# Kernel tuning notes

Measured on AMD Instinct MI355X. Metric: run time of the kernel, lower is better.

## Reference

```python
import jax, jax.numpy as jnp
import numpy as np
import math

B, T, C, N = 2, 2048, 1024, 16  # batch, seq, h_dim, n_heads
D = C // N                      # head dim = 64


def setup_inputs() -> dict:
    key = jax.random.key(0)
    ks = jax.random.split(key, 9)
    s = 1.0 / math.sqrt(C)
    x = jax.random.normal(ks[0], (B, T, C), dtype=jnp.float32)
    Wq = jax.random.normal(ks[1], (C, C), dtype=jnp.float32) * s
    Wk = jax.random.normal(ks[2], (C, C), dtype=jnp.float32) * s
    Wv = jax.random.normal(ks[3], (C, C), dtype=jnp.float32) * s
    Wp = jax.random.normal(ks[4], (C, C), dtype=jnp.float32) * s
    bq = jax.random.normal(ks[5], (C,), dtype=jnp.float32) * 0.01
    bk = jax.random.normal(ks[6], (C,), dtype=jnp.float32) * 0.01
    bv = jax.random.normal(ks[7], (C,), dtype=jnp.float32) * 0.01
    bp = jax.random.normal(ks[8], (C,), dtype=jnp.float32) * 0.01
    mask = jnp.tril(jnp.ones((T, T), dtype=jnp.int32))[None, None]  # [1,1,T,T] causal
    return {"x": x, "Wq": Wq, "bq": bq, "Wk": Wk, "bk": bk,
            "Wv": Wv, "bv": bv, "Wp": Wp, "bp": bp, "mask": mask}


def reference(x, Wq, bq, Wk, bk, Wv, bv, Wp, bp, mask):
    b, t, c = x.shape
    n, d = N, c // N
    # projections; rearrange 'b t (n d) -> b n t d'
    q = (x @ Wq + bq).reshape(b, t, n, d).transpose(0, 2, 1, 3)
    k = (x @ Wk + bk).reshape(b, t, n, d).transpose(0, 2, 1, 3)
    v = (x @ Wv + bv).reshape(b, t, n, d).transpose(0, 2, 1, 3)
    # source: (q @ k^T).transpose(2,3) -> weights[b,n,i,j] = q_j . k_i (TRANSPOSED scores)
    weights = jnp.einsum('bntd,bnsd->bnst', q, k) / math.sqrt(d)
    weights = jnp.where(mask == 0, -jnp.inf, weights)
    attn = jax.nn.softmax(weights, axis=-1)          # softmax over query index j
    out = jnp.einsum('bnij,bnjd->bnid', attn, v)     # [b,n,t,d]
    out = out.transpose(0, 2, 1, 3).reshape(b, t, c)
    return out @ Wp + bp
```

## Files before the change

kernel.cpp:

```cpp
#include <hip/hip_runtime.h>
#include <hip/hip_bf16.h>

#define TT 2048
#define NHD 16

typedef __attribute__((ext_vector_type(8))) short bf16x8;
typedef __attribute__((ext_vector_type(4))) float f32x4;
typedef __attribute__((ext_vector_type(8))) unsigned short us8;
typedef __attribute__((ext_vector_type(4))) unsigned short us4;

typedef __attribute__((address_space(1))) void gvoid;
typedef __attribute__((address_space(3))) void svoid;

__device__ __forceinline__ void gll16(const void* g, void* l) {
    __builtin_amdgcn_global_load_lds((gvoid*)g, (svoid*)l, 16, 0, 0);
}

__device__ __forceinline__ unsigned short f2bf(float f) {
    union { float f; unsigned u; } v; v.f = f;
    unsigned r = v.u + 0x7fffu + ((v.u >> 16) & 1u);
    return (unsigned short)(r >> 16);
}
__device__ __forceinline__ float bf2f(unsigned short u) {
    union { unsigned u; float f; } v; v.u = ((unsigned)u) << 16;
    return v.f;
}

#define MFMA16(a, b, c) __builtin_amdgcn_mfma_f32_16x16x32_bf16((a), (b), (c), 0, 0, 0)

__global__ __launch_bounds__(256) void convert_x(const float* __restrict__ x,
                                                 unsigned short* __restrict__ xh,
                                                 unsigned short* __restrict__ xl) {
    const int i = blockIdx.x * 256 + threadIdx.x;
    const float4 a = ((const float4*)x)[2 * i];
    const float4 b = ((const float4*)x)[2 * i + 1];
    const float v[8] = {a.x, a.y, a.z, a.w, b.x, b.y, b.z, b.w};
    us8 H, L;
    #pragma unroll
    for (int j = 0; j < 8; ++j) {
        const unsigned short h = f2bf(v[j]);
        H[j] = h;
        L[j] = f2bf(v[j] - bf2f(h));
    }
    ((us8*)xh)[i] = H;
    ((us8*)xl)[i] = L;
}

__global__ __launch_bounds__(256) void convert_w(const float* __restrict__ W,
                                                 unsigned short* __restrict__ Wh,
                                                 unsigned short* __restrict__ Wl) {
    __shared__ float tile[32 * 33];
    const int t = threadIdx.x;
    const int k0 = blockIdx.x * 32, n0 = blockIdx.y * 32;

    const int kl_ = t >> 3, nc = (t & 7) * 4;
    const float4 v = *(const float4*)&W[(size_t)(k0 + kl_) * 1024 + n0 + nc];
    tile[(nc + 0) * 33 + kl_] = v.x;
    tile[(nc + 1) * 33 + kl_] = v.y;
    tile[(nc + 2) * 33 + kl_] = v.z;
    tile[(nc + 3) * 33 + kl_] = v.w;
    __syncthreads();
    const int nl = t >> 3, kc = (t & 7) * 4;
    us4 H, L;
    #pragma unroll
    for (int j = 0; j < 4; ++j) {
        const float f = tile[nl * 33 + kc + j];
        const unsigned short h = f2bf(f);
        H[j] = h;
        L[j] = f2bf(f - bf2f(h));
    }
    *(us4*)&Wh[(size_t)(n0 + nl) * 1024 + k0 + kc] = H;
    *(us4*)&Wl[(size_t)(n0 + nl) * 1024 + k0 + kc] = L;
}

template <int OUTMODE>
__global__ __launch_bounds__(256, 3)
void proj_gemm(const unsigned short* __restrict__ Ah, const unsigned short* __restrict__ Al,
               const unsigned short* __restrict__ Bh, const unsigned short* __restrict__ Bl,
               const float* __restrict__ bias,
               unsigned short* __restrict__ Oh, unsigned short* __restrict__ Ol,
               float* __restrict__ Of) {
    __shared__ __align__(16) unsigned short sm[24576];
    unsigned short* sAh = sm;
    unsigned short* sAl = sm + 8192;
    unsigned short* sBh = sm + 16384;
    unsigned short* sBl = sm + 20480;

    const int t = threadIdx.x;
    const int lane = t & 63, w = t >> 6;
    const int wr = w >> 1, wc = w & 1;
    const int l15 = lane & 15, lq = lane >> 4;
    const int row0 = blockIdx.x * 128;
    const int col0 = blockIdx.y * 64;

    f32x4 acc[4][2] = {};

    for (int k0 = 0; k0 < 1024; k0 += 64) {
        __syncthreads();
        #pragma unroll
        for (int cc = 0; cc < 4; ++cc) {
            const int c = w * 4 + cc;
            const int r = 8 * c + (lane >> 3);
            const int src = (row0 + r) * 1024 + k0 + 8 * ((lane & 7) ^ (r & 7));
            gll16(&Ah[src], &sAh[c * 512]);
            gll16(&Al[src], &sAl[c * 512]);
        }
        #pragma unroll
        for (int cc = 0; cc < 2; ++cc) {
            const int c = w * 2 + cc;
            const int r = 8 * c + (lane >> 3);
            const int src = (col0 + r) * 1024 + k0 + 8 * ((lane & 7) ^ (r & 7));
            gll16(&Bh[src], &sBh[c * 512]);
            gll16(&Bl[src], &sBl[c * 512]);
        }
        __syncthreads();
        #pragma unroll
        for (int kh = 0; kh < 2; ++kh) {
            bf16x8 aH[4], aL[4], bH[2], bL[2];
            #pragma unroll
            for (int nt = 0; nt < 2; ++nt) {
                const int rn = 32 * wc + 16 * nt + l15;
                const int off = rn * 64 + 8 * ((lq + 4 * kh) ^ (rn & 7));
                bH[nt] = *(const bf16x8*)&sBh[off];
                bL[nt] = *(const bf16x8*)&sBl[off];
            }
            #pragma unroll
            for (int mt = 0; mt < 4; ++mt) {
                const int rm = 64 * wr + 16 * mt + l15;
                const int off = rm * 64 + 8 * ((lq + 4 * kh) ^ (rm & 7));
                aH[mt] = *(const bf16x8*)&sAh[off];
                aL[mt] = *(const bf16x8*)&sAl[off];
            }
            #pragma unroll
            for (int mt = 0; mt < 4; ++mt)
                #pragma unroll
                for (int nt = 0; nt < 2; ++nt) {
                    acc[mt][nt] = MFMA16(aH[mt], bH[nt], acc[mt][nt]);
                    acc[mt][nt] = MFMA16(aH[mt], bL[nt], acc[mt][nt]);
                    acc[mt][nt] = MFMA16(aL[mt], bH[nt], acc[mt][nt]);
                }
        }
    }

    __syncthreads();
    float* sc = (float*)sm + w * (64 * 36);
    #pragma unroll
    for (int mt = 0; mt < 4; ++mt)
        #pragma unroll
        for (int nt = 0; nt < 2; ++nt) {
            const float bsv = bias[col0 + 32 * wc + 16 * nt + l15];
            #pragma unroll
            for (int r = 0; r < 4; ++r)
                sc[(16 * mt + 4 * lq + r) * 36 + 16 * nt + l15] = acc[mt][nt][r] + bsv;
        }
    asm volatile("" ::: "memory");
    #pragma unroll
    for (int rr = 0; rr < 4; ++rr) {
        const int rl = 16 * rr + (lane >> 2);
        const int c8 = (lane & 3) * 8;
        const float4 f0 = *(const float4*)&sc[rl * 36 + c8];
        const float4 f1 = *(const float4*)&sc[rl * 36 + c8 + 4];
        const float v[8] = {f0.x, f0.y, f0.z, f0.w, f1.x, f1.y, f1.z, f1.w};
        const int gr = row0 + 64 * wr + rl;
        const int gc = col0 + 32 * wc + c8;
        if (OUTMODE == 2) {
            *(float4*)&Of[(size_t)gr * 1024 + gc] = f0;
            *(float4*)&Of[(size_t)gr * 1024 + gc + 4] = f1;
        } else {
            us8 H, L;
            #pragma unroll
            for (int j = 0; j < 8; ++j) {
                const unsigned short h = f2bf(v[j]);
                H[j] = h;
                L[j] = f2bf(v[j] - bf2f(h));
            }
            *(us8*)&Oh[(size_t)gr * 1024 + gc] = H;
            if (OUTMODE == 0) *(us8*)&Ol[(size_t)gr * 1024 + gc] = L;
        }
    }
}

__global__ __launch_bounds__(256, 3)
void attn_mfma(const unsigned short* __restrict__ Qh_, const unsigned short* __restrict__ Ql_,
               const unsigned short* __restrict__ Kh_, const unsigned short* __restrict__ Kl_,
               const unsigned short* __restrict__ Vh_,
               unsigned short* __restrict__ Oh, unsigned short* __restrict__ Ol) {
    __shared__ __align__(16) unsigned short sm[24576];
    unsigned short* sQh = sm;
    unsigned short* sQl = sm + 4096;
    unsigned short* sKh = sm + 8192;
    unsigned short* sKl = sm + 12288;
    unsigned short* sVt = sm + 16384;
    unsigned short* sP  = sm + 20480;

    const int t = threadIdx.x;
    const int lane = t & 63, w = t >> 6;
    const int l15 = lane & 15, lq = lane >> 4;
    const int bn = blockIdx.x;
    const int b = bn >> 4, n = bn & 15;
    const int qt = (gridDim.y - 1) - blockIdx.y;
    const int rowQ0 = b * TT + qt * 64;
    const int colh = n * 64;

    #pragma unroll
    for (int cc = 0; cc < 2; ++cc) {
        const int c = w * 2 + cc;
        const int r = 8 * c + (lane >> 3);
        const int src = (rowQ0 + r) * 1024 + colh + 8 * ((lane & 7) ^ (r & 7));
        gll16(&Qh_[src], &sQh[c * 512]);
        gll16(&Ql_[src], &sQl[c * 512]);
    }

    float m_[4], l_[4];
    f32x4 o[4] = {};
    #pragma unroll
    for (int r = 0; r < 4; ++r) { m_[r] = -1e30f; l_[r] = 0.f; }

    for (int kt = 0; kt <= qt; ++kt) {
        const int rowK0 = b * TT + kt * 64;
        __syncthreads();
        #pragma unroll
        for (int cc = 0; cc < 2; ++cc) {
            const int c = w * 2 + cc;
            const int r = 8 * c + (lane >> 3);
            const int src = (rowK0 + r) * 1024 + colh + 8 * ((lane & 7) ^ (r & 7));
            gll16(&Kh_[src], &sKh[c * 512]);
            gll16(&Kl_[src], &sKl[c * 512]);
        }
        {
            const int d = lane;
            unsigned pk[8];
            #pragma unroll
            for (int ip = 0; ip < 8; ++ip) {
                const int j0 = 16 * w + 2 * ip;
                const unsigned short v0 = Vh_[(rowK0 + j0) * 1024 + colh + d];
                const unsigned short v1 = Vh_[(rowK0 + j0 + 1) * 1024 + colh + d];
                pk[ip] = (unsigned)v0 | ((unsigned)v1 << 16);
            }
            unsigned* VtI = (unsigned*)sVt;
            #pragma unroll
            for (int ip = 0; ip < 8; ++ip) {
                const int slot = 2 * w + (ip >> 2);
                VtI[d * 32 + 4 * (slot ^ (d & 7)) + (ip & 3)] = pk[ip];
            }
        }
        __syncthreads();

        f32x4 s[4] = {};
        const int njt = (kt == qt) ? (w + 1) : 4;
        #pragma unroll
        for (int kh = 0; kh < 2; ++kh) {
            const int rq = 16 * w + l15;
            const int offq = rq * 64 + 8 * ((lq + 4 * kh) ^ (rq & 7));
            const bf16x8 qH = *(const bf16x8*)&sQh[offq];
            const bf16x8 qL = *(const bf16x8*)&sQl[offq];
            #pragma unroll
            for (int jt = 0; jt < 4; ++jt) {
                if (jt >= njt) continue;
                const int rk = 16 * jt + l15;
                const int offk = rk * 64 + 8 * ((lq + 4 * kh) ^ (rk & 7));
                const bf16x8 kH = *(const bf16x8*)&sKh[offk];
                const bf16x8 kL = *(const bf16x8*)&sKl[offk];
                s[jt] = MFMA16(qH, kH, s[jt]);
                s[jt] = MFMA16(qH, kL, s[jt]);
                s[jt] = MFMA16(qL, kH, s[jt]);
            }
        }
        if (kt == qt) {
            #pragma unroll
            for (int jt = 0; jt < 4; ++jt)
                #pragma unroll
                for (int r = 0; r < 4; ++r)
                    if (16 * jt + l15 > 16 * w + 4 * lq + r) s[jt][r] = -1e30f;
        }

        float po[4][4];
        #pragma unroll
        for (int r = 0; r < 4; ++r) {
            float mx = fmaxf(fmaxf(s[0][r], s[1][r]), fmaxf(s[2][r], s[3][r]));
            #pragma unroll
            for (int off = 8; off; off >>= 1) mx = fmaxf(mx, __shfl_xor(mx, off, 16));
            const float mnew = fmaxf(m_[r], mx);
            const float alpha = __expf((m_[r] - mnew) * 0.125f);
            m_[r] = mnew;
            float ps = 0.f;
            #pragma unroll
            for (int jt = 0; jt < 4; ++jt) {
                const float p = __expf((s[jt][r] - mnew) * 0.125f);
                po[r][jt] = p;
                ps += p;
            }
            #pragma unroll
            for (int off = 8; off; off >>= 1) ps += __shfl_xor(ps, off, 16);
            l_[r] = l_[r] * alpha + ps;
            #pragma unroll
            for (int dt = 0; dt < 4; ++dt) o[dt][r] *= alpha;
        }
        unsigned short* Pw = sP + w * 1024;
        #pragma unroll
        for (int r = 0; r < 4; ++r) {
            const int rl = 4 * lq + r;
            #pragma unroll
            for (int jt = 0; jt < 4; ++jt) {
                const int c = 16 * jt + l15;
                Pw[rl * 64 + 8 * ((c >> 3) ^ (rl & 7)) + (c & 7)] = f2bf(po[r][jt]);
            }
        }
        __syncthreads();

        #pragma unroll
        for (int kh = 0; kh < 2; ++kh) {
            const int offp = l15 * 64 + 8 * ((lq + 4 * kh) ^ (l15 & 7));
            const bf16x8 pa = *(const bf16x8*)&Pw[offp];
            #pragma unroll
            for (int dt = 0; dt < 4; ++dt) {
                const int rd = 16 * dt + l15;
                const int offv = rd * 64 + 8 * ((lq + 4 * kh) ^ (rd & 7));
                const bf16x8 vb = *(const bf16x8*)&sVt[offv];
                o[dt] = MFMA16(pa, vb, o[dt]);
            }
        }
    }

    float inv[4];
    #pragma unroll
    for (int r = 0; r < 4; ++r) inv[r] = 1.0f / l_[r];
    float* sc = (float*)sm + w * (16 * 68);
    #pragma unroll
    for (int dt = 0; dt < 4; ++dt)
        #pragma unroll
        for (int r = 0; r < 4; ++r)
            sc[(4 * lq + r) * 68 + 16 * dt + l15] = o[dt][r] * inv[r];
    asm volatile("" ::: "memory");
    #pragma unroll
    for (int it = 0; it < 2; ++it) {
        const int rl = 8 * it + (lane >> 3);
        const int c8 = (lane & 7) * 8;
        const float4 f0 = *(const float4*)&sc[rl * 68 + c8];
        const float4 f1 = *(const float4*)&sc[rl * 68 + c8 + 4];
        const float v[8] = {f0.x, f0.y, f0.z, f0.w, f1.x, f1.y, f1.z, f1.w};
        us8 H, L;
        #pragma unroll
        for (int j = 0; j < 8; ++j) {
            const unsigned short h = f2bf(v[j]);
            H[j] = h;
            L[j] = f2bf(v[j] - bf2f(h));
        }
        const int gt = rowQ0 + 16 * w + rl;
        *(us8*)&Oh[(size_t)gt * 1024 + colh + c8] = H;
        *(us8*)&Ol[(size_t)gt * 1024 + colh + c8] = L;
    }
}

extern "C" void kernel_launch(void* const* d_in, const int* in_sizes, int n_in,
                              void* d_out, int out_size, void* d_ws, size_t ws_size,
                              hipStream_t stream) {
    const float* x  = (const float*)d_in[0];
    const float* Wq = (const float*)d_in[1];
    const float* bq = (const float*)d_in[2];
    const float* Wk = (const float*)d_in[3];
    const float* bk = (const float*)d_in[4];
    const float* Wv = (const float*)d_in[5];
    const float* bv = (const float*)d_in[6];
    const float* Wp = (const float*)d_in[7];
    const float* bp = (const float*)d_in[8];
    float* out = (float*)d_out;

    char* p = (char*)d_ws;
    const size_t MB = 1024 * 1024;
    unsigned short* xh = (unsigned short*)(p);
    unsigned short* xl = (unsigned short*)(p + 8 * MB);
    unsigned short* qh = (unsigned short*)(p + 16 * MB);
    unsigned short* ql = (unsigned short*)(p + 24 * MB);
    unsigned short* kh = (unsigned short*)(p + 32 * MB);
    unsigned short* kl = (unsigned short*)(p + 40 * MB);
    unsigned short* vh = (unsigned short*)(p + 48 * MB);
    unsigned short* wh = (unsigned short*)(p + 56 * MB);
    unsigned short* wl = (unsigned short*)(p + 58 * MB);
    unsigned short* oh = xh;
    unsigned short* ol = xl;

    const dim3 blk(256);
    const dim3 gw(32, 32);
    const dim3 gp(32, 16);

    convert_x<<<2048, blk, 0, stream>>>(x, xh, xl);

    convert_w<<<gw, blk, 0, stream>>>(Wq, wh, wl);
    proj_gemm<0><<<gp, blk, 0, stream>>>(xh, xl, wh, wl, bq, qh, ql, nullptr);
    convert_w<<<gw, blk, 0, stream>>>(Wk, wh, wl);
    proj_gemm<0><<<gp, blk, 0, stream>>>(xh, xl, wh, wl, bk, kh, kl, nullptr);
    convert_w<<<gw, blk, 0, stream>>>(Wv, wh, wl);
    proj_gemm<1><<<gp, blk, 0, stream>>>(xh, xl, wh, wl, bv, vh, nullptr, nullptr);

    attn_mfma<<<dim3(32, 32), blk, 0, stream>>>(kh, kl, qh, ql, vh, oh, ol);

    convert_w<<<gw, blk, 0, stream>>>(Wp, wh, wl);
    proj_gemm<2><<<gp, blk, 0, stream>>>(oh, ol, wh, wl, bp, nullptr, nullptr, out);
}
```

Baseline: 300.1 us.

## Fuse Q/K projections, emit transposed V, and streamline attention softmax

Merges the Q and K projection GEMMs into one wider GEMM writing an interleaved QK buffer. The V projection now writes V pre-transposed per head, so attention can load it with async global-to-LDS copies instead of transposing it through registers. The GEMM is retiled to 128-column tiles with a K-step of 32, a block-id swizzle, and an XOR-swizzled epilogue. The attention kernel keeps Q in registers, reuses LDS for P to cut its footprint so more blocks fit per CU, adds MFMA priority hints, and skips the softmax rescale when the running max barely changes. The skip is a lazy-rescale bound that relies on the exponent not overflowing; it also adds complexity and raises register pressure.

Result: slower. 323.7 us (+7.9%).

```diff
diff --git a/kernel.cpp b/kernel.cpp
--- a/kernel.cpp
+++ b/kernel.cpp
@@ -2,7 +2,6 @@
 #include <hip/hip_bf16.h>
 
 #define TT 2048
-#define NHD 16
 
 typedef __attribute__((ext_vector_type(8))) short bf16x8;
 typedef __attribute__((ext_vector_type(4))) float f32x4;
@@ -73,125 +72,158 @@
     *(us4*)&Wl[(size_t)(n0 + nl) * 1024 + k0 + kc] = L;
 }
 
-template <int OUTMODE>
-__global__ __launch_bounds__(256, 3)
-void proj_gemm(const unsigned short* __restrict__ Ah, const unsigned short* __restrict__ Al,
-               const unsigned short* __restrict__ Bh, const unsigned short* __restrict__ Bl,
-               const float* __restrict__ bias,
-               unsigned short* __restrict__ Oh, unsigned short* __restrict__ Ol,
-               float* __restrict__ Of) {
-    __shared__ __align__(16) unsigned short sm[24576];
+template <int BM, int OUTMODE>
+__global__ __launch_bounds__(256, 2)
+void proj2(const unsigned short* __restrict__ Ah, const unsigned short* __restrict__ Al,
+           const unsigned short* __restrict__ Bh, const unsigned short* __restrict__ Bl,
+           const float* __restrict__ bias0, const float* __restrict__ bias1,
+           unsigned short* __restrict__ Oh, unsigned short* __restrict__ Ol,
+           float* __restrict__ Of) {
+    constexpr int MT = BM / 32;
+    constexpr int RW = BM / 2;
+    constexpr int CA = BM / 64;
+    __shared__ __align__(16) unsigned short sm[BM * 64 + 8192];
     unsigned short* sAh = sm;
-    unsigned short* sAl = sm + 8192;
-    unsigned short* sBh = sm + 16384;
-    unsigned short* sBl = sm + 20480;
+    unsigned short* sAl = sm + BM * 32;
+    unsigned short* sBh = sm + BM * 64;
+    unsigned short* sBl = sm + BM * 64 + 4096;
 
     const int t = threadIdx.x;
     const int lane = t & 63, w = t >> 6;
     const int wr = w >> 1, wc = w & 1;
     const int l15 = lane & 15, lq = lane >> 4;
-    const int row0 = blockIdx.x * 128;
-    const int col0 = blockIdx.y * 64;
-
-    f32x4 acc[4][2] = {};
-
-    for (int k0 = 0; k0 < 1024; k0 += 64) {
+
+    const int nwg = gridDim.x * gridDim.y;
+    const int bid = blockIdx.y * gridDim.x + blockIdx.x;
+    const int swz = (bid & 7) * (nwg >> 3) + (bid >> 3);
+    const int bx = swz % gridDim.x, by = swz / gridDim.x;
+    const int row0 = bx * BM;
+    const int col0 = by * 128;
+
+    f32x4 acc[MT][4] = {};
+
+    for (int k0 = 0; k0 < 1024; k0 += 32) {
         __syncthreads();
         #pragma unroll
-        for (int cc = 0; cc < 4; ++cc) {
-            const int c = w * 4 + cc;
-            const int r = 8 * c + (lane >> 3);
-            const int src = (row0 + r) * 1024 + k0 + 8 * ((lane & 7) ^ (r & 7));
+        for (int cc = 0; cc < CA; ++cc) {
+            const int c = w * CA + cc;
+            const int r = c * 16 + (lane >> 2);
+            const int src = (row0 + r) * 1024 + k0 + 8 * ((lane & 3) ^ ((r >> 1) & 3));
             gll16(&Ah[src], &sAh[c * 512]);
             gll16(&Al[src], &sAl[c * 512]);
         }
         #pragma unroll
         for (int cc = 0; cc < 2; ++cc) {
             const int c = w * 2 + cc;
-            const int r = 8 * c + (lane >> 3);
-            const int src = (col0 + r) * 1024 + k0 + 8 * ((lane & 7) ^ (r & 7));
+            const int r = c * 16 + (lane >> 2);
+            const int src = (col0 + r) * 1024 + k0 + 8 * ((lane & 3) ^ ((r >> 1) & 3));
             gll16(&Bh[src], &sBh[c * 512]);
             gll16(&Bl[src], &sBl[c * 512]);
         }
         __syncthreads();
-        #pragma unroll
-        for (int kh = 0; kh < 2; ++kh) {
-            bf16x8 aH[4], aL[4], bH[2], bL[2];
-            #pragma unroll
-            for (int nt = 0; nt < 2; ++nt) {
-                const int rn = 32 * wc + 16 * nt + l15;
-                const int off = rn * 64 + 8 * ((lq + 4 * kh) ^ (rn & 7));
-                bH[nt] = *(const bf16x8*)&sBh[off];
-                bL[nt] = *(const bf16x8*)&sBl[off];
-            }
-            #pragma unroll
-            for (int mt = 0; mt < 4; ++mt) {
-                const int rm = 64 * wr + 16 * mt + l15;
-                const int off = rm * 64 + 8 * ((lq + 4 * kh) ^ (rm & 7));
-                aH[mt] = *(const bf16x8*)&sAh[off];
-                aL[mt] = *(const bf16x8*)&sAl[off];
-            }
-            #pragma unroll
-            for (int mt = 0; mt < 4; ++mt)
-                #pragma unroll
-                for (int nt = 0; nt < 2; ++nt) {
-                    acc[mt][nt] = MFMA16(aH[mt], bH[nt], acc[mt][nt]);
-                    acc[mt][nt] = MFMA16(aH[mt], bL[nt], acc[mt][nt]);
-                    acc[mt][nt] = MFMA16(aL[mt], bH[nt], acc[mt][nt]);
+
+        bf16x8 aH[MT], aL[MT], bH[4], bL[4];
+        #pragma unroll
+        for (int nt = 0; nt < 4; ++nt) {
+            const int rn = 64 * wc + 16 * nt + l15;
+            const int off = rn * 32 + 8 * (lq ^ ((rn >> 1) & 3));
+            bH[nt] = *(const bf16x8*)&sBh[off];
+            bL[nt] = *(const bf16x8*)&sBl[off];
+        }
+        #pragma unroll
+        for (int mt = 0; mt < MT; ++mt) {
+            const int rm = RW * wr + 16 * mt + l15;
+            const int off = rm * 32 + 8 * (lq ^ ((rm >> 1) & 3));
+            aH[mt] = *(const bf16x8*)&sAh[off];
+            aL[mt] = *(const bf16x8*)&sAl[off];
+        }
+        #pragma unroll
+        for (int mt = 0; mt < MT; ++mt)
+            #pragma unroll
+            for (int nt = 0; nt < 4; ++nt) {
+                acc[mt][nt] = MFMA16(aH[mt], bH[nt], acc[mt][nt]);
+                acc[mt][nt] = MFMA16(aH[mt], bL[nt], acc[mt][nt]);
+                acc[mt][nt] = MFMA16(aL[mt], bH[nt], acc[mt][nt]);
+            }
+    }
+
+    if (OUTMODE == 3) {
+        #pragma unroll
+        for (int mt = 0; mt < MT; ++mt)
+            #pragma unroll
+            for (int nt = 0; nt < 4; ++nt) {
+                const int c = col0 + 64 * wc + 16 * nt + l15;
+                const float bb = bias0[c];
+                const int gr0 = row0 + RW * wr + 16 * mt + 4 * lq;
+                const int b = gr0 >> 11, t0 = gr0 & 2047;
+                us4 o4;
+                #pragma unroll
+                for (int r = 0; r < 4; ++r) o4[r] = f2bf(acc[mt][nt][r] + bb);
+                *(us4*)&Oh[((size_t)((b * 16 + (c >> 6)) * 64 + (c & 63))) * 2048 + t0] = o4;
+            }
+        return;
+    }
+
+    __syncthreads();
+    float* sc = (float*)sm + w * (RW * 32);
+    #pragma unroll
+    for (int h = 0; h < 2; ++h) {
+        #pragma unroll
+        for (int mt = 0; mt < MT; ++mt)
+            #pragma unroll
+            for (int nt2 = 0; nt2 < 2; ++nt2) {
+                const int nt = 2 * h + nt2;
+                const int colg = col0 + 64 * wc + 16 * nt + l15;
+                float bb;
+                if (OUTMODE == 0) bb = (col0 < 1024) ? bias0[colg] : bias1[colg - 1024];
+                else bb = bias0[colg];
+                const int cl = 16 * nt2 + l15;
+                #pragma unroll
+                for (int r = 0; r < 4; ++r) {
+                    const int row = 16 * mt + 4 * lq + r;
+                    sc[row * 32 + 4 * ((cl >> 2) ^ (row & 7)) + (cl & 3)] = acc[mt][nt][r] + bb;
                 }
-        }
-    }
-
-    __syncthreads();
-    float* sc = (float*)sm + w * (64 * 36);
-    #pragma unroll
-    for (int mt = 0; mt < 4; ++mt)
-        #pragma unroll
-        for (int nt = 0; nt < 2; ++nt) {
-            const float bsv = bias[col0 + 32 * wc + 16 * nt + l15];
-            #pragma unroll
-            for (int r = 0; r < 4; ++r)
-                sc[(16 * mt + 4 * lq + r) * 36 + 16 * nt + l15] = acc[mt][nt][r] + bsv;
-        }
-    asm volatile("" ::: "memory");
-    #pragma unroll
-    for (int rr = 0; rr < 4; ++rr) {
-        const int rl = 16 * rr + (lane >> 2);
-        const int c8 = (lane & 3) * 8;
-        const float4 f0 = *(const float4*)&sc[rl * 36 + c8];
-        const float4 f1 = *(const float4*)&sc[rl * 36 + c8 + 4];
-        const float v[8] = {f0.x, f0.y, f0.z, f0.w, f1.x, f1.y, f1.z, f1.w};
-        const int gr = row0 + 64 * wr + rl;
-        const int gc = col0 + 32 * wc + c8;
-        if (OUTMODE == 2) {
-            *(float4*)&Of[(size_t)gr * 1024 + gc] = f0;
-            *(float4*)&Of[(size_t)gr * 1024 + gc + 4] = f1;
-        } else {
-            us8 H, L;
-            #pragma unroll
-            for (int j = 0; j < 8; ++j) {
-                const unsigned short h = f2bf(v[j]);
-                H[j] = h;
-                L[j] = f2bf(v[j] - bf2f(h));
-            }
-            *(us8*)&Oh[(size_t)gr * 1024 + gc] = H;
-            if (OUTMODE == 0) *(us8*)&Ol[(size_t)gr * 1024 + gc] = L;
-        }
-    }
-}
-
-__global__ __launch_bounds__(256, 3)
-void attn_mfma(const unsigned short* __restrict__ Qh_, const unsigned short* __restrict__ Ql_,
-               const unsigned short* __restrict__ Kh_, const unsigned short* __restrict__ Kl_,
-               const unsigned short* __restrict__ Vh_,
-               unsigned short* __restrict__ Oh, unsigned short* __restrict__ Ol) {
-    __shared__ __align__(16) unsigned short sm[24576];
+            }
+        asm volatile("" ::: "memory");
+        #pragma unroll
+        for (int it = 0; it < RW / 16; ++it) {
+            const int rl = it * 16 + (lane >> 2);
+            const int c8 = (lane & 3) * 8;
+            const float4 f0 = *(const float4*)&sc[rl * 32 + 4 * ((c8 >> 2) ^ (rl & 7))];
+            const float4 f1 = *(const float4*)&sc[rl * 32 + 4 * (((c8 >> 2) + 1) ^ (rl & 7))];
+            const int gr = row0 + RW * wr + rl;
+            const int gc = col0 + 64 * wc + 32 * h + c8;
+            if (OUTMODE == 2) {
+                *(float4*)&Of[(size_t)gr * 1024 + gc] = f0;
+                *(float4*)&Of[(size_t)gr * 1024 + gc + 4] = f1;
+            } else {
+                const float v[8] = {f0.x, f0.y, f0.z, f0.w, f1.x, f1.y, f1.z, f1.w};
+                us8 H, L;
+                #pragma unroll
+                for (int j = 0; j < 8; ++j) {
+                    const unsigned short hh = f2bf(v[j]);
+                    H[j] = hh;
+                    L[j] = f2bf(v[j] - bf2f(hh));
+                }
+                *(us8*)&Oh[(size_t)gr * 2048 + gc] = H;
+                *(us8*)&Ol[(size_t)gr * 2048 + gc] = L;
+            }
+        }
+        asm volatile("" ::: "memory");
+    }
+}
+
+__global__ __launch_bounds__(256, 4)
+void attn2(const unsigned short* __restrict__ QKh, const unsigned short* __restrict__ QKl,
+           const unsigned short* __restrict__ Vt,
+           unsigned short* __restrict__ Oh, unsigned short* __restrict__ Ol) {
+    __shared__ __align__(16) unsigned short sm[20480];
     unsigned short* sQh = sm;
     unsigned short* sQl = sm + 4096;
     unsigned short* sKh = sm + 8192;
     unsigned short* sKl = sm + 12288;
     unsigned short* sVt = sm + 16384;
-    unsigned short* sP  = sm + 20480;
+    unsigned short* sP  = sm;
 
     const int t = threadIdx.x;
     const int lane = t & 63, w = t >> 6;
@@ -200,15 +232,25 @@
     const int b = bn >> 4, n = bn & 15;
     const int qt = (gridDim.y - 1) - blockIdx.y;
     const int rowQ0 = b * TT + qt * 64;
-    const int colh = n * 64;
+    const int colQ = 1024 + n * 64;
+    const int colK = n * 64;
 
     #pragma unroll
     for (int cc = 0; cc < 2; ++cc) {
         const int c = w * 2 + cc;
         const int r = 8 * c + (lane >> 3);
-        const int src = (rowQ0 + r) * 1024 + colh + 8 * ((lane & 7) ^ (r & 7));
-        gll16(&Qh_[src], &sQh[c * 512]);
-        gll16(&Ql_[src], &sQl[c * 512]);
+        const int src = (rowQ0 + r) * 2048 + colQ + 8 * ((lane & 7) ^ (r & 7));
+        gll16(&QKh[src], &sQh[c * 512]);
+        gll16(&QKl[src], &sQl[c * 512]);
+    }
+    __syncthreads();
+    bf16x8 qH[2], qL[2];
+    #pragma unroll
+    for (int kh = 0; kh < 2; ++kh) {
+        const int rq = 16 * w + l15;
+        const int off = rq * 64 + 8 * ((lq + 4 * kh) ^ (rq & 7));
+        qH[kh] = *(const bf16x8*)&sQh[off];
+        qL[kh] = *(const bf16x8*)&sQl[off];
     }
 
     float m_[4], l_[4];
@@ -223,37 +265,24 @@
         for (int cc = 0; cc < 2; ++cc) {
             const int c = w * 2 + cc;
             const int r = 8 * c + (lane >> 3);
-            const int src = (rowK0 + r) * 1024 + colh + 8 * ((lane & 7) ^ (r & 7));
-            gll16(&Kh_[src], &sKh[c * 512]);
-            gll16(&Kl_[src], &sKl[c * 512]);
-        }
-        {
-            const int d = lane;
-            unsigned pk[8];
-            #pragma unroll
-            for (int ip = 0; ip < 8; ++ip) {
-                const int j0 = 16 * w + 2 * ip;
-                const unsigned short v0 = Vh_[(rowK0 + j0) * 1024 + colh + d];
-                const unsigned short v1 = Vh_[(rowK0 + j0 + 1) * 1024 + colh + d];
-                pk[ip] = (unsigned)v0 | ((unsigned)v1 << 16);
-            }
-            unsigned* VtI = (unsigned*)sVt;
-            #pragma unroll
-            for (int ip = 0; ip < 8; ++ip) {
-                const int slot = 2 * w + (ip >> 2);
-                VtI[d * 32 + 4 * (slot ^ (d & 7)) + (ip & 3)] = pk[ip];
-            }
+            const int src = (rowK0 + r) * 2048 + colK + 8 * ((lane & 7) ^ (r & 7));
+            gll16(&QKh[src], &sKh[c * 512]);
+            gll16(&QKl[src], &sKl[c * 512]);
+        }
+        #pragma unroll
+        for (int cc = 0; cc < 2; ++cc) {
+            const int c = w * 2 + cc;
+            const int r = 8 * c + (lane >> 3);
+            const int src = (bn * 64 + r) * 2048 + kt * 64 + 8 * ((lane & 7) ^ (r & 7));
+            gll16(&Vt[src], &sVt[c * 512]);
         }
         __syncthreads();
 
         f32x4 s[4] = {};
         const int njt = (kt == qt) ? (w + 1) : 4;
+        __builtin_amdgcn_s_setprio(1);
         #pragma unroll
         for (int kh = 0; kh < 2; ++kh) {
-            const int rq = 16 * w + l15;
-            const int offq = rq * 64 + 8 * ((lq + 4 * kh) ^ (rq & 7));
-            const bf16x8 qH = *(const bf16x8*)&sQh[offq];
-            const bf16x8 qL = *(const bf16x8*)&sQl[offq];
             #pragma unroll
             for (int jt = 0; jt < 4; ++jt) {
                 if (jt >= njt) continue;
@@ -261,11 +290,12 @@
                 const int offk = rk * 64 + 8 * ((lq + 4 * kh) ^ (rk & 7));
                 const bf16x8 kH = *(const bf16x8*)&sKh[offk];
                 const bf16x8 kL = *(const bf16x8*)&sKl[offk];
-                s[jt] = MFMA16(qH, kH, s[jt]);
-                s[jt] = MFMA16(qH, kL, s[jt]);
-                s[jt] = MFMA16(qL, kH, s[jt]);
-            }
-        }
+                s[jt] = MFMA16(qH[kh], kH, s[jt]);
+                s[jt] = MFMA16(qH[kh], kL, s[jt]);
+                s[jt] = MFMA16(qL[kh], kH, s[jt]);
+            }
+        }
+        __builtin_amdgcn_s_setprio(0);
         if (kt == qt) {
             #pragma unroll
             for (int jt = 0; jt < 4; ++jt)
@@ -274,27 +304,50 @@
                     if (16 * jt + l15 > 16 * w + 4 * lq + r) s[jt][r] = -1e30f;
         }
 
+        float mx[4];
+        int need = 0;
+        #pragma unroll
+        for (int r = 0; r < 4; ++r) {
+            float m0 = fmaxf(fmaxf(s[0][r], s[1][r]), fmaxf(s[2][r], s[3][r]));
+            #pragma unroll
+            for (int off = 8; off; off >>= 1) m0 = fmaxf(m0, __shfl_xor(m0, off, 16));
+            mx[r] = m0;
+            need |= (m0 > m_[r] + 16.f) ? 1 : 0;
+        }
         float po[4][4];
-        #pragma unroll
-        for (int r = 0; r < 4; ++r) {
-            float mx = fmaxf(fmaxf(s[0][r], s[1][r]), fmaxf(s[2][r], s[3][r]));
-            #pragma unroll
-            for (int off = 8; off; off >>= 1) mx = fmaxf(mx, __shfl_xor(mx, off, 16));
-            const float mnew = fmaxf(m_[r], mx);
-            const float alpha = __expf((m_[r] - mnew) * 0.125f);
-            m_[r] = mnew;
-            float ps = 0.f;
-            #pragma unroll
-            for (int jt = 0; jt < 4; ++jt) {
-                const float p = __expf((s[jt][r] - mnew) * 0.125f);
-                po[r][jt] = p;
-                ps += p;
-            }
-            #pragma unroll
-            for (int off = 8; off; off >>= 1) ps += __shfl_xor(ps, off, 16);
-            l_[r] = l_[r] * alpha + ps;
-            #pragma unroll
-            for (int dt = 0; dt < 4; ++dt) o[dt][r] *= alpha;
+        if (__any(need)) {
+            #pragma unroll
+            for (int r = 0; r < 4; ++r) {
+                const float mnew = fmaxf(m_[r], mx[r]);
+                const float alpha = __expf((m_[r] - mnew) * 0.125f);
+                m_[r] = mnew;
+                float ps = 0.f;
+                #pragma unroll
+                for (int jt = 0; jt < 4; ++jt) {
+                    const float p = __expf((s[jt][r] - mnew) * 0.125f);
+                    po[r][jt] = p;
+                    ps += p;
+                }
+                #pragma unroll
+                for (int off = 8; off; off >>= 1) ps += __shfl_xor(ps, off, 16);
+                l_[r] = l_[r] * alpha + ps;
+                #pragma unroll
+                for (int dt = 0; dt < 4; ++dt) o[dt][r] *= alpha;
+            }
+        } else {
+            #pragma unroll
+            for (int r = 0; r < 4; ++r) {
+                float ps = 0.f;
+                #pragma unroll
+                for (int jt = 0; jt < 4; ++jt) {
+                    const float p = __expf((s[jt][r] - m_[r]) * 0.125f);
+                    po[r][jt] = p;
+                    ps += p;
+                }
+                #pragma unroll
+                for (int off = 8; off; off >>= 1) ps += __shfl_xor(ps, off, 16);
+                l_[r] += ps;
+            }
         }
         unsigned short* Pw = sP + w * 1024;
         #pragma unroll
@@ -308,6 +361,7 @@
         }
         __syncthreads();
 
+        __builtin_amdgcn_s_setprio(1);
         #pragma unroll
         for (int kh = 0; kh < 2; ++kh) {
             const int offp = l15 * 64 + 8 * ((lq + 4 * kh) ^ (l15 & 7));
@@ -320,8 +374,10 @@
                 o[dt] = MFMA16(pa, vb, o[dt]);
             }
         }
-    }
-
+        __builtin_amdgcn_s_setprio(0);
+    }
+
+    __syncthreads();
     float inv[4];
     #pragma unroll
     for (int r = 0; r < 4; ++r) inv[r] = 1.0f / l_[r];
@@ -347,8 +403,8 @@
             L[j] = f2bf(v[j] - bf2f(h));
         }
         const int gt = rowQ0 + 16 * w + rl;
-        *(us8*)&Oh[(size_t)gt * 1024 + colh + c8] = H;
-        *(us8*)&Ol[(size_t)gt * 1024 + colh + c8] = L;
+        *(us8*)&Oh[(size_t)gt * 1024 + (n * 64) + c8] = H;
+        *(us8*)&Ol[(size_t)gt * 1024 + (n * 64) + c8] = L;
     }
 }
 
@@ -368,33 +424,34 @@
 
     char* p = (char*)d_ws;
     const size_t MB = 1024 * 1024;
-    unsigned short* xh = (unsigned short*)(p);
-    unsigned short* xl = (unsigned short*)(p + 8 * MB);
-    unsigned short* qh = (unsigned short*)(p + 16 * MB);
-    unsigned short* ql = (unsigned short*)(p + 24 * MB);
-    unsigned short* kh = (unsigned short*)(p + 32 * MB);
-    unsigned short* kl = (unsigned short*)(p + 40 * MB);
-    unsigned short* vh = (unsigned short*)(p + 48 * MB);
-    unsigned short* wh = (unsigned short*)(p + 56 * MB);
-    unsigned short* wl = (unsigned short*)(p + 58 * MB);
+    unsigned short* xh  = (unsigned short*)(p);
+    unsigned short* xl  = (unsigned short*)(p +  8 * MB);
+    unsigned short* qkh = (unsigned short*)(p + 16 * MB);
+    unsigned short* qkl = (unsigned short*)(p + 32 * MB);
+    unsigned short* vh  = (unsigned short*)(p + 48 * MB);
+    unsigned short* wbh = (unsigned short*)(p + 56 * MB);
+    unsigned short* wbl = (unsigned short*)(p + 60 * MB);
+    unsigned short* wsh = (unsigned short*)(p + 56 * MB);
+    unsigned short* wsl = (unsigned short*)(p + 58 * MB);
     unsigned short* oh = xh;
     unsigned short* ol = xl;
 
     const dim3 blk(256);
     const dim3 gw(32, 32);
-    const dim3 gp(32, 16);
 
     convert_x<<<2048, blk, 0, stream>>>(x, xh, xl);
 
-    convert_w<<<gw, blk, 0, stream>>>(Wq, wh, wl);
-    proj_gemm<0><<<gp, blk, 0, stream>>>(xh, xl, wh, wl, bq, qh, ql, nullptr);
-    convert_w<<<gw, blk, 0, stream>>>(Wk, wh, wl);
-    proj_gemm<0><<<gp, blk, 0, stream>>>(xh, xl, wh, wl, bk, kh, kl, nullptr);
-    convert_w<<<gw, blk, 0, stream>>>(Wv, wh, wl);
-    proj_gemm<1><<<gp, blk, 0, stream>>>(xh, xl, wh, wl, bv, vh, nullptr, nullptr);
-
-    attn_mfma<<<dim3(32, 32), blk, 0, stream>>>(kh, kl, qh, ql, vh, oh, ol);
-
-    convert_w<<<gw, blk, 0, stream>>>(Wp, wh, wl);
-    proj_gemm<2><<<gp, blk, 0, stream>>>(oh, ol, wh, wl, bp, nullptr, nullptr, out);
-}
+    convert_w<<<gw, blk, 0, stream>>>(Wq, wbh, wbl);
+    convert_w<<<gw, blk, 0, stream>>>(Wk, wbh + 1024 * 1024, wbl + 1024 * 1024);
+    proj2<128, 0><<<dim3(32, 16), blk, 0, stream>>>(xh, xl, wbh, wbl, bq, bk,
+                                                    qkh, qkl, nullptr);
+    convert_w<<<gw, blk, 0, stream>>>(Wv, wsh, wsl);
+    proj2<64, 3><<<dim3(64, 8), blk, 0, stream>>>(xh, xl, wsh, wsl, bv, nullptr,
+                                                  vh, nullptr, nullptr);
+
+    attn2<<<dim3(32, 32), blk, 0, stream>>>(qkh, qkl, vh, oh, ol);
+
+    convert_w<<<gw, blk, 0, stream>>>(Wp, wsh, wsl);
+    proj2<64, 2><<<dim3(64, 8), blk, 0, stream>>>(oh, ol, wsh, wsl, bp, nullptr,
+                                                  nullptr, nullptr, out);
+}
```
